# Kernel tuning notes

Measured on AMD Instinct MI355X. Metric: run time of the kernel, lower is better.

## Reference

```python
import jax, jax.numpy as jnp
import numpy as np

B = 2_000_000
IN, HID = 5, 4


def setup_inputs() -> dict:
    key = jax.random.key(0)
    ks = jax.random.split(key, 16)
    f = lambda k, shp: (jax.random.normal(k, shp, dtype=jnp.float32) * 0.3)
    inp = {
        "xl": jax.random.normal(ks[0], (B, IN), dtype=jnp.float32),
        "yl": jax.random.normal(ks[1], (B, IN), dtype=jnp.float32),
        "xr": jax.random.normal(ks[2], (B, IN), dtype=jnp.float32),
        "yr": jax.random.normal(ks[3], (B, IN), dtype=jnp.float32),
        # 6 stacked branches, order: [lxl, lyl, lxr, lyr, rxl, ryl]
        "W1": f(ks[4], (6, HID, IN)),
        "b1": f(ks[5], (6, HID)),
        "W2": f(ks[6], (6, HID, HID)),
        "b2": f(ks[7], (6, HID)),
        # fc3 with 2 outputs, order: [lxl, lyl, rxl, ryl] (branch idx 0,1,4,5)
        "W3_2": f(ks[8], (4, 2, HID)),
        "b3_2": f(ks[9], (4, 2)),
        # fc3 with 1 output, order: [lxr, lyr] (branch idx 2,3)
        "W3_1": f(ks[10], (2, 1, HID)),
        "b3_1": f(ks[11], (2, 1)),
        # fc4, order: [xl, yl]
        "W4": f(ks[12], (2, 1, HID)),
        "b4": f(ks[13], (2, 1)),
    }
    return inp


def reference(xl, yl, xr, yr, W1, b1, W2, b2, W3_2, b3_2, W3_1, b3_1, W4, b4):
    # Stack the six branch inputs: [6, B, 5]. NOTE: fc_1lyr consumes yl (yr unused),
    # faithful to the original forward.
    X = jnp.stack([xl, yl, xr, yl, xl, yl], axis=0)
    h1 = jax.nn.sigmoid(jnp.einsum("kbi,khi->kbh", X, W1) + b1[:, None, :])
    h2 = jax.nn.sigmoid(jnp.einsum("kbh,kgh->kbg", h1, W2) + b2[:, None, :])
    # fc3 heads with 2 outputs: branches lxl(0), lyl(1), rxl(4), ryl(5)
    h2_2 = h2[jnp.array([0, 1, 4, 5])]                       # [4, B, 4]
    o2 = jnp.einsum("kbh,koh->kbo", h2_2, W3_2) + b3_2[:, None, :]  # [4, B, 2]
    # fc3 heads with 1 output: branches lxr(2), lyr(3)
    h2_1 = h2[jnp.array([2, 3])]                             # [2, B, 4]
    o1 = jnp.einsum("kbh,koh->kbo", h2_1, W3_1) + b3_1[:, None, :]  # [2, B, 1]
    # concat (per-sample dim, was dim=0 unbatched)
    out_xl = jnp.concatenate([o2[0], o2[2]], axis=-1)        # [B, 4]
    out_yl = jnp.concatenate([o2[1], o2[3]], axis=-1)        # [B, 4]
    fc4xl = out_xl @ W4[0].T + b4[0]                         # [B, 1]
    fc4yl = out_yl @ W4[1].T + b4[1]                         # [B, 1]
    out = jnp.concatenate([o1[0], o1[1], fc4xl, fc4yl], axis=-1)  # [B, 4]
    return out
```

## Files before the change

### kernel.cpp

```cpp
#include <hip/hip_runtime.h>

#define NTHREADS 256
#define SPT 2

__device__ __forceinline__ float fast_sigmoid(float x) {
    return __builtin_amdgcn_rcpf(1.0f + __expf(-x));
}

__global__ __launch_bounds__(NTHREADS, 4)
void mlp6_fused_kernel(const float* __restrict__ xl,
                       const float* __restrict__ yl,
                       const float* __restrict__ xr,
                       const float* __restrict__ W1, const float* __restrict__ b1,
                       const float* __restrict__ W2, const float* __restrict__ b2,
                       const float* __restrict__ W3_2, const float* __restrict__ b3_2,
                       const float* __restrict__ W3_1, const float* __restrict__ b3_1,
                       const float* __restrict__ W4, const float* __restrict__ b4,
                       float* __restrict__ out, int B)
{
    __shared__ __align__(16) float w[296];
    const int tid = threadIdx.x;

    for (int t = tid; t < 292; t += NTHREADS) {
        float v;
        if (t < 264) {
            int k = t / 44, r = t % 44;
            if (r < 20)      v = W1[k*20 + r];
            else if (r < 24) v = b1[k*4 + (r-20)];
            else if (r < 40) v = W2[k*16 + (r-24)];
            else             v = b2[k*4 + (r-40)];
            w[k*48 + r] = v;
        } else if (t < 288) {
            int q = t - 264, k = q >> 2, h = q & 3;
            if (k == 0)      v = W4[0]*W3_2[h]     + W4[1]*W3_2[4+h];
            else if (k == 1) v = W4[4]*W3_2[8+h]   + W4[5]*W3_2[12+h];
            else if (k == 2) v = W3_1[h];
            else if (k == 3) v = W3_1[4+h];
            else if (k == 4) v = W4[2]*W3_2[16+h]  + W4[3]*W3_2[20+h];
            else             v = W4[6]*W3_2[24+h]  + W4[7]*W3_2[28+h];
            w[k*48 + 44 + h] = v;
        } else {
            int j = t - 288;
            if (j == 0)      v = b3_1[0];
            else if (j == 1) v = b3_1[1];
            else if (j == 2) v = W4[0]*b3_2[0] + W4[1]*b3_2[1] + W4[2]*b3_2[4] + W4[3]*b3_2[5] + b4[0];
            else             v = W4[4]*b3_2[2] + W4[5]*b3_2[3] + W4[6]*b3_2[6] + W4[7]*b3_2[7] + b4[1];
            w[288 + j] = v;
        }
    }
    __syncthreads();

    const float fb0 = w[288], fb1 = w[289], fb2 = w[290], fb3 = w[291];

    long long base = (long long)blockIdx.x * (NTHREADS * SPT) + tid;
    long long idx[SPT];
    #pragma unroll
    for (int s = 0; s < SPT; s++) {
        long long i = base + (long long)s * NTHREADS;
        idx[s] = (i < B) ? i : (long long)(B - 1);
    }

    float xs[SPT][15];
    #pragma unroll
    for (int s = 0; s < SPT; s++) {
        long long p = idx[s] * 5;
        #pragma unroll
        for (int j = 0; j < 5; j++) {
            xs[s][j]      = xl[p + j];
            xs[s][5 + j]  = yl[p + j];
            xs[s][10 + j] = xr[p + j];
        }
    }

    float o[SPT][4];
    #pragma unroll
    for (int s = 0; s < SPT; s++) { o[s][0]=fb0; o[s][1]=fb1; o[s][2]=fb2; o[s][3]=fb3; }

    constexpr int xoff[6] = {0, 5, 10, 5, 0, 5};
    constexpr int oidx[6] = {2, 3, 0, 1, 2, 3};

    #pragma unroll
    for (int k = 0; k < 6; k++) {
        float wk[48];
        const float4* w4p = (const float4*)&w[k*48];
        #pragma unroll
        for (int q = 0; q < 12; q++) {
            float4 t4 = w4p[q];
            wk[q*4+0]=t4.x; wk[q*4+1]=t4.y; wk[q*4+2]=t4.z; wk[q*4+3]=t4.w;
        }
        #pragma unroll
        for (int s = 0; s < SPT; s++) {
            float h1[4];
            #pragma unroll
            for (int h = 0; h < 4; h++) {
                float a = wk[20+h];
                #pragma unroll
                for (int i = 0; i < 5; i++) a = fmaf(xs[s][xoff[k]+i], wk[h*5+i], a);
                h1[h] = fast_sigmoid(a);
            }
            float h2[4];
            #pragma unroll
            for (int g = 0; g < 4; g++) {
                float a = wk[40+g];
                #pragma unroll
                for (int h = 0; h < 4; h++) a = fmaf(h1[h], wk[24+g*4+h], a);
                h2[g] = fast_sigmoid(a);
            }
            float c = 0.0f;
            #pragma unroll
            for (int h = 0; h < 4; h++) c = fmaf(h2[h], wk[44+h], c);
            o[s][oidx[k]] += c;
        }
    }

    #pragma unroll
    for (int s = 0; s < SPT; s++) {
        float4 r; r.x = o[s][0]; r.y = o[s][1]; r.z = o[s][2]; r.w = o[s][3];
        ((float4*)out)[idx[s]] = r;
    }
}

extern "C" void kernel_launch(void* const* d_in, const int* in_sizes, int n_in,
                              void* d_out, int out_size, void* d_ws, size_t ws_size,
                              hipStream_t stream) {
    const float* xl   = (const float*)d_in[0];
    const float* yl   = (const float*)d_in[1];
    const float* xr   = (const float*)d_in[2];
    const float* W1   = (const float*)d_in[4];
    const float* b1   = (const float*)d_in[5];
    const float* W2   = (const float*)d_in[6];
    const float* b2   = (const float*)d_in[7];
    const float* W3_2 = (const float*)d_in[8];
    const float* b3_2 = (const float*)d_in[9];
    const float* W3_1 = (const float*)d_in[10];
    const float* b3_1 = (const float*)d_in[11];
    const float* W4   = (const float*)d_in[12];
    const float* b4   = (const float*)d_in[13];
    float* out = (float*)d_out;

    int B = in_sizes[0] / 5;
    int blocks = (B + NTHREADS * SPT - 1) / (NTHREADS * SPT);
    mlp6_fused_kernel<<<blocks, NTHREADS, 0, stream>>>(
        xl, yl, xr, W1, b1, W2, b2, W3_2, b3_2, W3_1, b3_1, W4, b4, out, B);
}
```

Before: 42.42 us.

## Process four contiguous samples per thread with float4 loads and scalar weights

Each thread now handles four consecutive samples, so each input array is read as five aligned float4 loads instead of scattered scalar loads. The shared-memory weight staging and block barrier are removed. Weights are read from global memory with uniform indices, and readfirstlane is applied to the folded head weights so they can live in scalar registers. Sigmoid now uses a hardware exp2 intrinsic. The tail only works when B is a multiple of four, since B>>2 silently drops any remainder samples.

```diff
diff --git a/kernel.cpp b/kernel.cpp
--- a/kernel.cpp
+++ b/kernel.cpp
@@ -1,10 +1,24 @@
 #include <hip/hip_runtime.h>
 
 #define NTHREADS 256
-#define SPT 2
 
-__device__ __forceinline__ float fast_sigmoid(float x) {
-    return __builtin_amdgcn_rcpf(1.0f + __expf(-x));
+#if defined(__has_builtin)
+#if __has_builtin(__builtin_amdgcn_exp2f)
+#define EXP2F __builtin_amdgcn_exp2f
+#else
+#define EXP2F exp2f
+#endif
+#else
+#define EXP2F exp2f
+#endif
+
+__device__ __forceinline__ float rfl(float x) {
+    return __uint_as_float(__builtin_amdgcn_readfirstlane(__float_as_uint(x)));
+}
+
+__device__ __forceinline__ float sigm(float a) {
+    float e = EXP2F(a * -1.442695040888963f);
+    return __builtin_amdgcn_rcpf(1.0f + e);
 }
 
 __global__ __launch_bounds__(NTHREADS, 4)
@@ -18,105 +32,99 @@
                        const float* __restrict__ W4, const float* __restrict__ b4,
                        float* __restrict__ out, int B)
 {
-    __shared__ __align__(16) float w[296];
     const int tid = threadIdx.x;
+    const long long nq = (long long)(B >> 2);
+    long long gq = (long long)blockIdx.x * NTHREADS + tid;
+    if (gq >= nq) gq = nq - 1;
 
-    for (int t = tid; t < 292; t += NTHREADS) {
-        float v;
-        if (t < 264) {
-            int k = t / 44, r = t % 44;
-            if (r < 20)      v = W1[k*20 + r];
-            else if (r < 24) v = b1[k*4 + (r-20)];
-            else if (r < 40) v = W2[k*16 + (r-24)];
-            else             v = b2[k*4 + (r-40)];
-            w[k*48 + r] = v;
-        } else if (t < 288) {
-            int q = t - 264, k = q >> 2, h = q & 3;
-            if (k == 0)      v = W4[0]*W3_2[h]     + W4[1]*W3_2[4+h];
-            else if (k == 1) v = W4[4]*W3_2[8+h]   + W4[5]*W3_2[12+h];
-            else if (k == 2) v = W3_1[h];
-            else if (k == 3) v = W3_1[4+h];
-            else if (k == 4) v = W4[2]*W3_2[16+h]  + W4[3]*W3_2[20+h];
-            else             v = W4[6]*W3_2[24+h]  + W4[7]*W3_2[28+h];
-            w[k*48 + 44 + h] = v;
-        } else {
-            int j = t - 288;
-            if (j == 0)      v = b3_1[0];
-            else if (j == 1) v = b3_1[1];
-            else if (j == 2) v = W4[0]*b3_2[0] + W4[1]*b3_2[1] + W4[2]*b3_2[4] + W4[3]*b3_2[5] + b4[0];
-            else             v = W4[4]*b3_2[2] + W4[5]*b3_2[3] + W4[6]*b3_2[6] + W4[7]*b3_2[7] + b4[1];
-            w[288 + j] = v;
-        }
-    }
-    __syncthreads();
-
-    const float fb0 = w[288], fb1 = w[289], fb2 = w[290], fb3 = w[291];
-
-    long long base = (long long)blockIdx.x * (NTHREADS * SPT) + tid;
-    long long idx[SPT];
-    #pragma unroll
-    for (int s = 0; s < SPT; s++) {
-        long long i = base + (long long)s * NTHREADS;
-        idx[s] = (i < B) ? i : (long long)(B - 1);
-    }
-
-    float xs[SPT][15];
-    #pragma unroll
-    for (int s = 0; s < SPT; s++) {
-        long long p = idx[s] * 5;
+    float bl[20], by[20], br_[20];
+    {
+        const float4* a4 = (const float4*)xl;
+        const float4* y4 = (const float4*)yl;
+        const float4* c4 = (const float4*)xr;
+        long long p = gq * 5;
         #pragma unroll
-        for (int j = 0; j < 5; j++) {
-            xs[s][j]      = xl[p + j];
-            xs[s][5 + j]  = yl[p + j];
-            xs[s][10 + j] = xr[p + j];
+        for (int q = 0; q < 5; q++) {
+            ((float4*)bl)[q]  = a4[p + q];
+            ((float4*)by)[q]  = y4[p + q];
+            ((float4*)br_)[q] = c4[p + q];
         }
     }
 
-    float o[SPT][4];
+    float fw[6][4];
     #pragma unroll
-    for (int s = 0; s < SPT; s++) { o[s][0]=fb0; o[s][1]=fb1; o[s][2]=fb2; o[s][3]=fb3; }
+    for (int h = 0; h < 4; h++) {
+        fw[0][h] = rfl(fmaf(W4[1], W3_2[4 + h],  W4[0] * W3_2[h]));
+        fw[1][h] = rfl(fmaf(W4[5], W3_2[12 + h], W4[4] * W3_2[8 + h]));
+        fw[2][h] = rfl(W3_1[h]);
+        fw[3][h] = rfl(W3_1[4 + h]);
+        fw[4][h] = rfl(fmaf(W4[3], W3_2[20 + h], W4[2] * W3_2[16 + h]));
+        fw[5][h] = rfl(fmaf(W4[7], W3_2[28 + h], W4[6] * W3_2[24 + h]));
+    }
+    float fbv[4];
+    fbv[0] = rfl(b3_1[0]);
+    fbv[1] = rfl(b3_1[1]);
+    fbv[2] = rfl(W4[0]*b3_2[0] + W4[1]*b3_2[1] + W4[2]*b3_2[4] + W4[3]*b3_2[5] + b4[0]);
+    fbv[3] = rfl(W4[4]*b3_2[2] + W4[5]*b3_2[3] + W4[6]*b3_2[6] + W4[7]*b3_2[7] + b4[1]);
 
-    constexpr int xoff[6] = {0, 5, 10, 5, 0, 5};
-    constexpr int oidx[6] = {2, 3, 0, 1, 2, 3};
+    float o[4][4];
+    #pragma unroll
+    for (int s = 0; s < 4; s++) {
+        #pragma unroll
+        for (int j = 0; j < 4; j++) o[s][j] = fbv[j];
+    }
 
-    #pragma unroll
-    for (int k = 0; k < 6; k++) {
-        float wk[48];
-        const float4* w4p = (const float4*)&w[k*48];
+    auto branch = [&](int k, const float* xb, int slot) {
+        float h1[4][4];
         #pragma unroll
-        for (int q = 0; q < 12; q++) {
-            float4 t4 = w4p[q];
-            wk[q*4+0]=t4.x; wk[q*4+1]=t4.y; wk[q*4+2]=t4.z; wk[q*4+3]=t4.w;
+        for (int h = 0; h < 4; h++) {
+            float a[4];
+            float bb = b1[k*4 + h];
+            #pragma unroll
+            for (int s = 0; s < 4; s++) a[s] = bb;
+            #pragma unroll
+            for (int i = 0; i < 5; i++) {
+                float wv = W1[k*20 + h*5 + i];
+                #pragma unroll
+                for (int s = 0; s < 4; s++) a[s] = fmaf(xb[s*5 + i], wv, a[s]);
+            }
+            #pragma unroll
+            for (int s = 0; s < 4; s++) h1[s][h] = sigm(a[s]);
+        }
+        float c[4] = {0.f, 0.f, 0.f, 0.f};
+        #pragma unroll
+        for (int g = 0; g < 4; g++) {
+            float a[4];
+            float bb = b2[k*4 + g];
+            #pragma unroll
+            for (int s = 0; s < 4; s++) a[s] = bb;
+            #pragma unroll
+            for (int h = 0; h < 4; h++) {
+                float wv = W2[k*16 + g*4 + h];
+                #pragma unroll
+                for (int s = 0; s < 4; s++) a[s] = fmaf(h1[s][h], wv, a[s]);
+            }
+            float fg = fw[k][g];
+            #pragma unroll
+            for (int s = 0; s < 4; s++) c[s] = fmaf(sigm(a[s]), fg, c[s]);
         }
         #pragma unroll
-        for (int s = 0; s < SPT; s++) {
-            float h1[4];
-            #pragma unroll
-            for (int h = 0; h < 4; h++) {
-                float a = wk[20+h];
-                #pragma unroll
-                for (int i = 0; i < 5; i++) a = fmaf(xs[s][xoff[k]+i], wk[h*5+i], a);
-                h1[h] = fast_sigmoid(a);
-            }
-            float h2[4];
-            #pragma unroll
-            for (int g = 0; g < 4; g++) {
-                float a = wk[40+g];
-                #pragma unroll
-                for (int h = 0; h < 4; h++) a = fmaf(h1[h], wk[24+g*4+h], a);
-                h2[g] = fast_sigmoid(a);
-            }
-            float c = 0.0f;
-            #pragma unroll
-            for (int h = 0; h < 4; h++) c = fmaf(h2[h], wk[44+h], c);
-            o[s][oidx[k]] += c;
-        }
-    }
+        for (int s = 0; s < 4; s++) o[s][slot] += c[s];
+    };
 
+    branch(0, bl, 2);
+    branch(4, bl, 2);
+    branch(1, by, 3);
+    branch(3, by, 1);
+    branch(5, by, 3);
+    branch(2, br_, 0);
+
+    float4* out4 = (float4*)out;
     #pragma unroll
-    for (int s = 0; s < SPT; s++) {
-        float4 r; r.x = o[s][0]; r.y = o[s][1]; r.z = o[s][2]; r.w = o[s][3];
-        ((float4*)out)[idx[s]] = r;
+    for (int s = 0; s < 4; s++) {
+        float4 r;
+        r.x = o[s][0]; r.y = o[s][1]; r.z = o[s][2]; r.w = o[s][3];
+        out4[gq*4 + s] = r;
     }
 }
 
@@ -139,7 +147,8 @@
     float* out = (float*)d_out;
 
     int B = in_sizes[0] / 5;
-    int blocks = (B + NTHREADS * SPT - 1) / (NTHREADS * SPT);
+    long long nq = (long long)B >> 2;
+    int blocks = (int)((nq + NTHREADS - 1) / NTHREADS);
     mlp6_fused_kernel<<<blocks, NTHREADS, 0, stream>>>(
         xl, yl, xr, W1, b1, W2, b2, W3_2, b3_2, W3_1, b3_1, W4, b4, out, B);
 }
```

New measurement: 42.85 us. Within noise of the previous version (+1.0%).
